# Performance work log

Hardware: AMD Instinct MI355X
Metric: run time of the kernel (lower is better)

The kernel has to match this reference:

```python
import jax, jax.numpy as jnp
import numpy as np

ENCODER_DIM, DECODER_DIM, ATTENTION_DIM = 2048, 512, 512
B, L = 128, 196


def setup_inputs() -> dict:
    key = jax.random.key(0)
    ks = jax.random.split(key, 8)
    s_u = 1.0 / np.sqrt(ENCODER_DIM)
    s_w = 1.0 / np.sqrt(DECODER_DIM)
    s_a = 1.0 / np.sqrt(ATTENTION_DIM)
    return {
        "features": jax.random.normal(ks[0], (B, L, ENCODER_DIM), jnp.float32),
        "hidden_state": jax.random.normal(ks[1], (B, DECODER_DIM), jnp.float32),
        "U_w": jax.random.uniform(ks[2], (ENCODER_DIM, ATTENTION_DIM), jnp.float32, -s_u, s_u),
        "U_b": jax.random.uniform(ks[3], (ATTENTION_DIM,), jnp.float32, -s_u, s_u),
        "W_w": jax.random.uniform(ks[4], (DECODER_DIM, ATTENTION_DIM), jnp.float32, -s_w, s_w),
        "W_b": jax.random.uniform(ks[5], (ATTENTION_DIM,), jnp.float32, -s_w, s_w),
        "A_w": jax.random.uniform(ks[6], (ATTENTION_DIM,), jnp.float32, -s_a, s_a),
        "A_b": jax.random.uniform(ks[7], (1,), jnp.float32, -s_a, s_a),
    }


def reference(features, hidden_state, U_w, U_b, W_w, W_b, A_w, A_b):
    # u_hs: [B, L, A], w_ah: [B, A]
    u_hs = jnp.einsum('ble,ea->bla', features, U_w) + U_b
    w_ah = hidden_state @ W_w + W_b
    combined = jnp.tanh(u_hs + w_ah[:, None, :])          # [B, L, A]
    scores = jnp.einsum('bla,a->bl', combined, A_w) + A_b[0]  # [B, L]
    alpha = jax.nn.softmax(scores, axis=1)                 # [B, L]
    context = jnp.einsum('bl,ble->be', alpha, features)    # [B, E]
    return alpha, context
```

## Files before the change

### kernel.cpp

```cpp
#include <hip/hip_runtime.h>
#include <hip/hip_bf16.h>

#define ENC 2048
#define ADIM 512
#define DEC 512
#define NBATCH 128
#define NL 196
#define MTOT (NBATCH * NL)
#define NKT 32

typedef __attribute__((ext_vector_type(8))) short short8;
typedef __attribute__((ext_vector_type(4))) float f32x4;
typedef __attribute__((ext_vector_type(4))) unsigned int u32x4;

__device__ __forceinline__ unsigned short f2bf(float f) {
    __hip_bfloat16 h = __float2bfloat16(f);
    union { __hip_bfloat16 h; unsigned short u; } cv; cv.h = h; return cv.u;
}
__device__ __forceinline__ unsigned int f2bf2(float lo, float hi) {
    __hip_bfloat162 h = __float22bfloat162_rn(float2{lo, hi});
    union { __hip_bfloat162 h; unsigned int u; } cv; cv.h = h; return cv.u;
}

__device__ __forceinline__ void load_lds16(const void* g, void* l) {
    __builtin_amdgcn_global_load_lds(
        (const __attribute__((address_space(1))) unsigned int*)g,
        (__attribute__((address_space(3))) unsigned int*)l, 16, 0, 0);
}

__global__ void wah_kernel(const float* __restrict__ hidden, const float* __restrict__ Ww,
                           const float* __restrict__ Wb, float* __restrict__ wah) {
    __shared__ __align__(16) float hs[DEC];
    const int b = blockIdx.x, a = threadIdx.x;
    hs[a] = hidden[b * DEC + a];
    __syncthreads();
    float acc = Wb[a];
    #pragma unroll 4
    for (int d = 0; d < DEC; d += 4) {
        f32x4 h = *(const f32x4*)&hs[d];
        acc += h.x * Ww[(d    ) * ADIM + a];
        acc += h.y * Ww[(d + 1) * ADIM + a];
        acc += h.z * Ww[(d + 2) * ADIM + a];
        acc += h.w * Ww[(d + 3) * ADIM + a];
    }
    wah[b * ADIM + a] = acc;
}

__global__ void transpose_uw(const float* __restrict__ Uw, unsigned short* __restrict__ uwT) {
    __shared__ float t[32][33];
    const int k0 = blockIdx.x * 32, n0 = blockIdx.y * 32;
    const int tx = threadIdx.x, ty = threadIdx.y;
    #pragma unroll
    for (int i = 0; i < 4; ++i)
        t[ty + 8 * i][tx] = Uw[(size_t)(k0 + ty + 8 * i) * ADIM + n0 + tx];
    __syncthreads();
    #pragma unroll
    for (int i = 0; i < 4; ++i)
        uwT[(size_t)(n0 + ty + 8 * i) * ENC + k0 + tx] = f2bf(t[tx][ty + 8 * i]);
}

__global__ __launch_bounds__(256, 3) void gemm_score(
    const float* __restrict__ feat, const unsigned short* __restrict__ uwT,
    const float* __restrict__ Ub, const float* __restrict__ wahb,
    const float* __restrict__ Aw, float* __restrict__ part)
{
    __shared__ __align__(16) unsigned char As[32768];
    __shared__ __align__(16) unsigned char Bs[16384];

    const int tid  = threadIdx.x;
    const int lane = tid & 63;
    const int w    = tid >> 6;
    const int wr   = w >> 1, wc = w & 1;
    const int l15  = lane & 15, ldr = lane >> 4;

    const int bid  = blockIdx.x;
    const int work = (bid & 7) * 98 + (bid >> 3);
    const int mb   = work >> 2;
    const int nbk  = work & 3;

    const float* aS[8];
    #pragma unroll
    for (int c = 0; c < 8; ++c) {
        const int rowc = c * 4 + ldr;
        const int sslot = l15 ^ (rowc & 15);
        aS[c] = feat + (size_t)(mb * 128 + w * 32 + rowc) * ENC + sslot * 4;
    }
    const int swzB = ((lane & 7) ^ ((lane >> 3) & 7)) << 3;
    const unsigned short* bS = uwT + (size_t)(nbk * 128 + w * 32 + (lane >> 3)) * ENC + swzB;

    int abyte[4][2][2];
    int bbyte[4][2];
    #pragma unroll
    for (int f = 0; f < 4; ++f) {
        const int ra = wr * 64 + f * 16 + l15;
        const int rb = wc * 64 + f * 16 + l15;
        #pragma unroll
        for (int ks = 0; ks < 2; ++ks) {
            abyte[f][ks][0] = ra * 256 + (((ks * 8 + ldr * 2 + 0) ^ l15) << 4);
            abyte[f][ks][1] = ra * 256 + (((ks * 8 + ldr * 2 + 1) ^ l15) << 4);
            bbyte[f][ks]    = rb * 128 + (((ks * 4 + ldr) ^ (rb & 7)) << 4);
        }
    }

    f32x4 acc[4][4];
    #pragma unroll
    for (int i = 0; i < 4; ++i)
        #pragma unroll
        for (int j = 0; j < 4; ++j)
            acc[i][j] = (f32x4){0.f, 0.f, 0.f, 0.f};

    #pragma unroll 1
    for (int kt = 0; kt < NKT; ++kt) {
        #pragma unroll
        for (int c = 0; c < 8; ++c)
            load_lds16(aS[c] + (size_t)kt * 64, As + w * 8192 + c * 1024);
        #pragma unroll
        for (int c = 0; c < 4; ++c)
            load_lds16(bS + (size_t)kt * 64 + c * 8 * ENC, Bs + w * 4096 + c * 1024);
        __syncthreads();

        #pragma unroll
        for (int ks = 0; ks < 2; ++ks) {
            short8 af[4], bf[4];
            #pragma unroll
            for (int f = 0; f < 4; ++f) {
                f32x4 lo = *(const f32x4*)(As + abyte[f][ks][0]);
                f32x4 hi = *(const f32x4*)(As + abyte[f][ks][1]);
                union { unsigned int u[4]; short8 s; } cv;
                cv.u[0] = f2bf2(lo.x, lo.y);
                cv.u[1] = f2bf2(lo.z, lo.w);
                cv.u[2] = f2bf2(hi.x, hi.y);
                cv.u[3] = f2bf2(hi.z, hi.w);
                af[f] = cv.s;
                bf[f] = *(const short8*)(Bs + bbyte[f][ks]);
            }
            #pragma unroll
            for (int fm = 0; fm < 4; ++fm)
                #pragma unroll
                for (int fn = 0; fn < 4; ++fn)
                    acc[fm][fn] = __builtin_amdgcn_mfma_f32_16x16x32_bf16(
                        af[fm], bf[fn], acc[fm][fn], 0, 0, 0);
        }
        __syncthreads();
    }

    float ub4[4], aw4[4]; int cidx[4];
    #pragma unroll
    for (int f = 0; f < 4; ++f) {
        const int c = nbk * 128 + wc * 64 + f * 16 + l15;
        cidx[f] = c; ub4[f] = Ub[c]; aw4[f] = Aw[c];
    }
    #pragma unroll
    for (int fm = 0; fm < 4; ++fm) {
        #pragma unroll
        for (int r = 0; r < 4; ++r) {
            const int m = mb * 128 + wr * 64 + fm * 16 + ldr * 4 + r;
            const int b = m / NL;
            const float* wrow = wahb + b * ADIM;
            float s = 0.f;
            #pragma unroll
            for (int f = 0; f < 4; ++f)
                s += aw4[f] * tanhf(acc[fm][f][r] + ub4[f] + wrow[cidx[f]]);
            s += __shfl_xor(s, 1);
            s += __shfl_xor(s, 2);
            s += __shfl_xor(s, 4);
            s += __shfl_xor(s, 8);
            if (l15 == 0) part[(nbk * 2 + wc) * MTOT + m] = s;
        }
    }
}

__global__ void softmax_kernel(const float* __restrict__ part, const float* __restrict__ Ab,
                               float* __restrict__ alpha) {
    const int b = blockIdx.x, t = threadIdx.x;
    float sv = 0.f;
    if (t < NL) {
        sv = Ab[0];
        #pragma unroll
        for (int p = 0; p < 8; ++p) sv += part[p * MTOT + b * NL + t];
    }
    float v = (t < NL) ? sv : -3.4e38f;
    #pragma unroll
    for (int o = 32; o >= 1; o >>= 1) v = fmaxf(v, __shfl_xor(v, o));
    __shared__ float rm[4], rs[4];
    if ((t & 63) == 0) rm[t >> 6] = v;
    __syncthreads();
    const float bm = fmaxf(fmaxf(rm[0], rm[1]), fmaxf(rm[2], rm[3]));
    const float e = (t < NL) ? expf(sv - bm) : 0.f;
    float s = e;
    #pragma unroll
    for (int o = 32; o >= 1; o >>= 1) s += __shfl_xor(s, o);
    if ((t & 63) == 0) rs[t >> 6] = s;
    __syncthreads();
    const float bs = rs[0] + rs[1] + rs[2] + rs[3];
    if (t < NL) alpha[b * NL + t] = e / bs;
}

__global__ void context_kernel(const float* __restrict__ feat, const float* __restrict__ alpha,
                               float* __restrict__ ctx) {
    __shared__ float al[NL];
    const int b = blockIdx.x, chunk = blockIdx.y, t = threadIdx.x;
    for (int i = t; i < NL; i += 128) al[i] = alpha[b * NL + i];
    __syncthreads();
    const int e0 = chunk * 512 + t * 4;
    const float* fp = feat + (size_t)b * NL * ENC + e0;
    f32x4 acc0 = (f32x4){0.f, 0.f, 0.f, 0.f};
    f32x4 acc1 = (f32x4){0.f, 0.f, 0.f, 0.f};
    #pragma unroll 2
    for (int l = 0; l < NL; l += 2) {
        f32x4 f0 = *(const f32x4*)(fp + (size_t)l * ENC);
        f32x4 f1 = *(const f32x4*)(fp + (size_t)(l + 1) * ENC);
        acc0 += al[l] * f0;
        acc1 += al[l + 1] * f1;
    }
    f32x4 rsum = acc0 + acc1;
    *(f32x4*)(ctx + (size_t)b * ENC + e0) = rsum;
}

extern "C" void kernel_launch(void* const* d_in, const int* in_sizes, int n_in,
                              void* d_out, int out_size, void* d_ws, size_t ws_size,
                              hipStream_t stream) {
    const float* feat   = (const float*)d_in[0];
    const float* hidden = (const float*)d_in[1];
    const float* Uw     = (const float*)d_in[2];
    const float* Ub     = (const float*)d_in[3];
    const float* Ww     = (const float*)d_in[4];
    const float* Wb     = (const float*)d_in[5];
    const float* Aw     = (const float*)d_in[6];
    const float* Ab     = (const float*)d_in[7];

    float* out   = (float*)d_out;
    float* alpha = out;
    float* ctx   = out + MTOT;

    char* ws = (char*)d_ws;
    float*          wahb  = (float*)ws;
    unsigned short* uwT   = (unsigned short*)(ws + 262144);
    float*          partb = (float*)(ws + 262144 + 2097152);

    wah_kernel<<<dim3(128), dim3(512), 0, stream>>>(hidden, Ww, Wb, wahb);
    transpose_uw<<<dim3(64, 16), dim3(32, 8), 0, stream>>>(Uw, uwT);
    gemm_score<<<dim3(784), dim3(256), 0, stream>>>(feat, uwT, Ub, wahb, Aw, partb);
    softmax_kernel<<<dim3(128), dim3(256), 0, stream>>>(partb, Ab, alpha);
    context_kernel<<<dim3(128, 4), dim3(128), 0, stream>>>(feat, alpha, ctx);
}
```

Before: 187.7 us.

## Compute full attention width per block to read features once

The score GEMM now uses 512-thread blocks that each cover all 512 attention columns for 128 rows, instead of four blocks per row tile. This removes the fourfold re-reading and fp32-to-bf16 conversion of the feature rows. The per-column partial scores are reduced in shared memory, so the softmax reads a single score array. The trade-off is fewer blocks (196) than compute units, larger LDS use and higher accumulator register pressure.

```diff
diff --git a/kernel.cpp b/kernel.cpp
--- a/kernel.cpp
+++ b/kernel.cpp
@@ -59,126 +59,117 @@
         uwT[(size_t)(n0 + ty + 8 * i) * ENC + k0 + tx] = f2bf(t[tx][ty + 8 * i]);
 }
 
-__global__ __launch_bounds__(256, 3) void gemm_score(
+__global__ __launch_bounds__(512, 2) void gemm_score512(
     const float* __restrict__ feat, const unsigned short* __restrict__ uwT,
     const float* __restrict__ Ub, const float* __restrict__ wahb,
-    const float* __restrict__ Aw, float* __restrict__ part)
+    const float* __restrict__ Aw, float* __restrict__ scores)
 {
     __shared__ __align__(16) unsigned char As[32768];
-    __shared__ __align__(16) unsigned char Bs[16384];
+    __shared__ __align__(16) unsigned char Bs[65536];
+    __shared__ float sred[4][128];
 
     const int tid  = threadIdx.x;
     const int lane = tid & 63;
     const int w    = tid >> 6;
-    const int wr   = w >> 1, wc = w & 1;
+    const int wr   = w >> 2;
+    const int wc   = w & 3;
     const int l15  = lane & 15, ldr = lane >> 4;
-
-    const int bid  = blockIdx.x;
-    const int work = (bid & 7) * 98 + (bid >> 3);
-    const int mb   = work >> 2;
-    const int nbk  = work & 3;
-
-    const float* aS[8];
-    #pragma unroll
-    for (int c = 0; c < 8; ++c) {
+    const int mb   = blockIdx.x;
+
+    const float* aS[4];
+    #pragma unroll
+    for (int c = 0; c < 4; ++c) {
         const int rowc = c * 4 + ldr;
-        const int sslot = l15 ^ (rowc & 15);
-        aS[c] = feat + (size_t)(mb * 128 + w * 32 + rowc) * ENC + sslot * 4;
-    }
-    const int swzB = ((lane & 7) ^ ((lane >> 3) & 7)) << 3;
-    const unsigned short* bS = uwT + (size_t)(nbk * 128 + w * 32 + (lane >> 3)) * ENC + swzB;
-
-    int abyte[4][2][2];
-    int bbyte[4][2];
-    #pragma unroll
-    for (int f = 0; f < 4; ++f) {
-        const int ra = wr * 64 + f * 16 + l15;
-        const int rb = wc * 64 + f * 16 + l15;
-        #pragma unroll
-        for (int ks = 0; ks < 2; ++ks) {
-            abyte[f][ks][0] = ra * 256 + (((ks * 8 + ldr * 2 + 0) ^ l15) << 4);
-            abyte[f][ks][1] = ra * 256 + (((ks * 8 + ldr * 2 + 1) ^ l15) << 4);
-            bbyte[f][ks]    = rb * 128 + (((ks * 4 + ldr) ^ (rb & 7)) << 4);
-        }
-    }
-
-    f32x4 acc[4][4];
+        aS[c] = feat + (size_t)(mb * 128 + w * 16 + rowc) * ENC + ((l15 ^ rowc) << 2);
+    }
+    const unsigned short* bS = uwT
+        + (size_t)(w * 64 + (lane >> 3)) * ENC
+        + (((lane & 7) ^ ((lane >> 3) & 7)) << 3);
+
+    f32x4 acc[4][8];
     #pragma unroll
     for (int i = 0; i < 4; ++i)
         #pragma unroll
-        for (int j = 0; j < 4; ++j)
+        for (int j = 0; j < 8; ++j)
             acc[i][j] = (f32x4){0.f, 0.f, 0.f, 0.f};
+
+    const int aRowBase = (wr * 64 + l15) * 256;
+    const int bRowBase = (wc * 128 + l15) * 128;
 
     #pragma unroll 1
     for (int kt = 0; kt < NKT; ++kt) {
         #pragma unroll
+        for (int c = 0; c < 4; ++c)
+            load_lds16(aS[c] + (size_t)kt * 64, As + w * 4096 + c * 1024);
+        #pragma unroll
         for (int c = 0; c < 8; ++c)
-            load_lds16(aS[c] + (size_t)kt * 64, As + w * 8192 + c * 1024);
-        #pragma unroll
-        for (int c = 0; c < 4; ++c)
-            load_lds16(bS + (size_t)kt * 64 + c * 8 * ENC, Bs + w * 4096 + c * 1024);
+            load_lds16(bS + (size_t)kt * 64 + c * 8 * ENC, Bs + w * 8192 + c * 1024);
         __syncthreads();
 
         #pragma unroll
         for (int ks = 0; ks < 2; ++ks) {
-            short8 af[4], bf[4];
+            short8 af[4];
             #pragma unroll
             for (int f = 0; f < 4; ++f) {
-                f32x4 lo = *(const f32x4*)(As + abyte[f][ks][0]);
-                f32x4 hi = *(const f32x4*)(As + abyte[f][ks][1]);
+                const int q0 = (ks * 8 + ldr * 2) ^ l15;
+                const int q1 = (ks * 8 + ldr * 2 + 1) ^ l15;
+                f32x4 lo = *(const f32x4*)(As + aRowBase + f * 4096 + (q0 << 4));
+                f32x4 hi = *(const f32x4*)(As + aRowBase + f * 4096 + (q1 << 4));
                 union { unsigned int u[4]; short8 s; } cv;
                 cv.u[0] = f2bf2(lo.x, lo.y);
                 cv.u[1] = f2bf2(lo.z, lo.w);
                 cv.u[2] = f2bf2(hi.x, hi.y);
                 cv.u[3] = f2bf2(hi.z, hi.w);
                 af[f] = cv.s;
-                bf[f] = *(const short8*)(Bs + bbyte[f][ks]);
             }
+            const int bSlot = (((ks * 4 + ldr) ^ (l15 & 7)) << 4);
             #pragma unroll
-            for (int fm = 0; fm < 4; ++fm)
+            for (int fn = 0; fn < 8; ++fn) {
+                short8 bf = *(const short8*)(Bs + bRowBase + fn * 2048 + bSlot);
                 #pragma unroll
-                for (int fn = 0; fn < 4; ++fn)
+                for (int fm = 0; fm < 4; ++fm)
                     acc[fm][fn] = __builtin_amdgcn_mfma_f32_16x16x32_bf16(
-                        af[fm], bf[fn], acc[fm][fn], 0, 0, 0);
+                        af[fm], bf, acc[fm][fn], 0, 0, 0);
+            }
         }
         __syncthreads();
     }
 
-    float ub4[4], aw4[4]; int cidx[4];
-    #pragma unroll
-    for (int f = 0; f < 4; ++f) {
-        const int c = nbk * 128 + wc * 64 + f * 16 + l15;
-        cidx[f] = c; ub4[f] = Ub[c]; aw4[f] = Aw[c];
+    float ub8[8], aw8[8]; int cidx[8];
+    #pragma unroll
+    for (int fn = 0; fn < 8; ++fn) {
+        const int c = wc * 128 + fn * 16 + l15;
+        cidx[fn] = c; ub8[fn] = Ub[c]; aw8[fn] = Aw[c];
     }
     #pragma unroll
     for (int fm = 0; fm < 4; ++fm) {
         #pragma unroll
         for (int r = 0; r < 4; ++r) {
-            const int m = mb * 128 + wr * 64 + fm * 16 + ldr * 4 + r;
-            const int b = m / NL;
+            const int lr = wr * 64 + fm * 16 + ldr * 4 + r;
+            const int m  = mb * 128 + lr;
+            const int b  = m / NL;
             const float* wrow = wahb + b * ADIM;
             float s = 0.f;
             #pragma unroll
-            for (int f = 0; f < 4; ++f)
-                s += aw4[f] * tanhf(acc[fm][f][r] + ub4[f] + wrow[cidx[f]]);
+            for (int fn = 0; fn < 8; ++fn)
+                s += aw8[fn] * tanhf(acc[fm][fn][r] + ub8[fn] + wrow[cidx[fn]]);
             s += __shfl_xor(s, 1);
             s += __shfl_xor(s, 2);
             s += __shfl_xor(s, 4);
             s += __shfl_xor(s, 8);
-            if (l15 == 0) part[(nbk * 2 + wc) * MTOT + m] = s;
+            if (l15 == 0) sred[wc][lr] = s;
         }
     }
-}
-
-__global__ void softmax_kernel(const float* __restrict__ part, const float* __restrict__ Ab,
+    __syncthreads();
+    if (tid < 128)
+        scores[mb * 128 + tid] = sred[0][tid] + sred[1][tid] + sred[2][tid] + sred[3][tid];
+}
+
+__global__ void softmax_kernel(const float* __restrict__ scores, const float* __restrict__ Ab,
                                float* __restrict__ alpha) {
     const int b = blockIdx.x, t = threadIdx.x;
     float sv = 0.f;
-    if (t < NL) {
-        sv = Ab[0];
-        #pragma unroll
-        for (int p = 0; p < 8; ++p) sv += part[p * MTOT + b * NL + t];
-    }
+    if (t < NL) sv = scores[b * NL + t] + Ab[0];
     float v = (t < NL) ? sv : -3.4e38f;
     #pragma unroll
     for (int o = 32; o >= 1; o >>= 1) v = fmaxf(v, __shfl_xor(v, o));
@@ -234,13 +225,13 @@
     float* ctx   = out + MTOT;
 
     char* ws = (char*)d_ws;
-    float*          wahb  = (float*)ws;
-    unsigned short* uwT   = (unsigned short*)(ws + 262144);
-    float*          partb = (float*)(ws + 262144 + 2097152);
+    float*          wahb   = (float*)ws;
+    unsigned short* uwT    = (unsigned short*)(ws + 262144);
+    float*          scores = (float*)(ws + 262144 + 2097152);
 
     wah_kernel<<<dim3(128), dim3(512), 0, stream>>>(hidden, Ww, Wb, wahb);
     transpose_uw<<<dim3(64, 16), dim3(32, 8), 0, stream>>>(Uw, uwT);
-    gemm_score<<<dim3(784), dim3(256), 0, stream>>>(feat, uwT, Ub, wahb, Aw, partb);
-    softmax_kernel<<<dim3(128), dim3(256), 0, stream>>>(partb, Ab, alpha);
+    gemm_score512<<<dim3(196), dim3(512), 0, stream>>>(feat, uwT, Ub, wahb, Aw, scores);
+    softmax_kernel<<<dim3(128), dim3(256), 0, stream>>>(scores, Ab, alpha);
     context_kernel<<<dim3(128, 4), dim3(128), 0, stream>>>(feat, alpha, ctx);
 }
```

New measurement: 167.7 us. -10.7%, faster.

## Pre-convert features to bf16 and double-buffer the score GEMM pipeline

Applied to the files above, without the earlier changes.

Adds a pass that converts the feature tensor to bf16 once, so the score GEMM loads bf16 directly into LDS instead of converting fp32 per tile. The GEMM is restructured into a two-stage double-buffered K loop with smaller LDS tiles and higher occupancy. The context reduction reads the bf16 copy, halving its bytes but lowering its precision. The extra conversion pass adds a full read plus half-size write of features, and the context kernel launches fewer blocks.

```diff
diff --git a/kernel.cpp b/kernel.cpp
--- a/kernel.cpp
+++ b/kernel.cpp
@@ -7,7 +7,7 @@
 #define NBATCH 128
 #define NL 196
 #define MTOT (NBATCH * NL)
-#define NKT 32
+#define NK32 64
 
 typedef __attribute__((ext_vector_type(8))) short short8;
 typedef __attribute__((ext_vector_type(4))) float f32x4;
@@ -20,12 +20,29 @@
 __device__ __forceinline__ unsigned int f2bf2(float lo, float hi) {
     __hip_bfloat162 h = __float22bfloat162_rn(float2{lo, hi});
     union { __hip_bfloat162 h; unsigned int u; } cv; cv.h = h; return cv.u;
+}
+__device__ __forceinline__ float bf2f(unsigned short u) {
+    union { unsigned int u; float f; } cv; cv.u = ((unsigned int)u) << 16; return cv.f;
 }
 
 __device__ __forceinline__ void load_lds16(const void* g, void* l) {
     __builtin_amdgcn_global_load_lds(
         (const __attribute__((address_space(1))) unsigned int*)g,
         (__attribute__((address_space(3))) unsigned int*)l, 16, 0, 0);
+}
+
+__global__ void cvt_feat_kernel(const float* __restrict__ feat, unsigned short* __restrict__ featb) {
+    const size_t total  = (size_t)MTOT * ENC;
+    const size_t stride = (size_t)gridDim.x * blockDim.x * 8;
+    size_t i = ((size_t)blockIdx.x * blockDim.x + threadIdx.x) * 8;
+    for (; i < total; i += stride) {
+        f32x4 lo = *(const f32x4*)(feat + i);
+        f32x4 hi = *(const f32x4*)(feat + i + 4);
+        u32x4 v;
+        v.x = f2bf2(lo.x, lo.y); v.y = f2bf2(lo.z, lo.w);
+        v.z = f2bf2(hi.x, hi.y); v.w = f2bf2(hi.z, hi.w);
+        *(u32x4*)(featb + i) = v;
+    }
 }
 
 __global__ void wah_kernel(const float* __restrict__ hidden, const float* __restrict__ Ww,
@@ -59,13 +76,15 @@
         uwT[(size_t)(n0 + ty + 8 * i) * ENC + k0 + tx] = f2bf(t[tx][ty + 8 * i]);
 }
 
-__global__ __launch_bounds__(256, 3) void gemm_score(
-    const float* __restrict__ feat, const unsigned short* __restrict__ uwT,
+__global__ __launch_bounds__(256, 4) void gemm_score_2ph(
+    const unsigned short* __restrict__ featb, const unsigned short* __restrict__ uwT,
     const float* __restrict__ Ub, const float* __restrict__ wahb,
     const float* __restrict__ Aw, float* __restrict__ part)
 {
-    __shared__ __align__(16) unsigned char As[32768];
-    __shared__ __align__(16) unsigned char Bs[16384];
+    __shared__ __align__(16) unsigned char Ab0[8192];
+    __shared__ __align__(16) unsigned char Ab1[8192];
+    __shared__ __align__(16) unsigned char Bb0[8192];
+    __shared__ __align__(16) unsigned char Bb1[8192];
 
     const int tid  = threadIdx.x;
     const int lane = tid & 63;
@@ -78,28 +97,19 @@
     const int mb   = work >> 2;
     const int nbk  = work & 3;
 
-    const float* aS[8];
-    #pragma unroll
-    for (int c = 0; c < 8; ++c) {
-        const int rowc = c * 4 + ldr;
-        const int sslot = l15 ^ (rowc & 15);
-        aS[c] = feat + (size_t)(mb * 128 + w * 32 + rowc) * ENC + sslot * 4;
-    }
-    const int swzB = ((lane & 7) ^ ((lane >> 3) & 7)) << 3;
-    const unsigned short* bS = uwT + (size_t)(nbk * 128 + w * 32 + (lane >> 3)) * ENC + swzB;
-
-    int abyte[4][2][2];
-    int bbyte[4][2];
+    const int srow  = lane >> 2;
+    const int sslot = (lane & 3) ^ ((lane >> 3) & 3);
+    const unsigned short* aS = featb + (size_t)(mb  * 128 + w * 32 + srow) * ENC + sslot * 8;
+    const unsigned short* bS = uwT   + (size_t)(nbk * 128 + w * 32 + srow) * ENC + sslot * 8;
+
+    const int rs = (l15 >> 1) & 3;
+    int abyte[4], bbyte[4];
     #pragma unroll
     for (int f = 0; f < 4; ++f) {
         const int ra = wr * 64 + f * 16 + l15;
         const int rb = wc * 64 + f * 16 + l15;
-        #pragma unroll
-        for (int ks = 0; ks < 2; ++ks) {
-            abyte[f][ks][0] = ra * 256 + (((ks * 8 + ldr * 2 + 0) ^ l15) << 4);
-            abyte[f][ks][1] = ra * 256 + (((ks * 8 + ldr * 2 + 1) ^ l15) << 4);
-            bbyte[f][ks]    = rb * 128 + (((ks * 4 + ldr) ^ (rb & 7)) << 4);
-        }
+        abyte[f] = ra * 64 + ((ldr ^ rs) << 4);
+        bbyte[f] = rb * 64 + ((ldr ^ rs) << 4);
     }
 
     f32x4 acc[4][4];
@@ -109,40 +119,47 @@
         for (int j = 0; j < 4; ++j)
             acc[i][j] = (f32x4){0.f, 0.f, 0.f, 0.f};
 
+#define STAGE(KT, AB, BB) {                                                   \
+    _Pragma("unroll")                                                         \
+    for (int c = 0; c < 2; ++c) {                                             \
+        load_lds16(aS + (size_t)(KT) * 32 + c * 16 * ENC,                     \
+                   (AB) + w * 2048 + c * 1024);                               \
+        load_lds16(bS + (size_t)(KT) * 32 + c * 16 * ENC,                     \
+                   (BB) + w * 2048 + c * 1024);                               \
+    }                                                                         \
+    __builtin_amdgcn_sched_barrier(0);                                        \
+}
+#define COMPUTE(AB, BB) {                                                     \
+    short8 af[4], bf[4];                                                      \
+    _Pragma("unroll")                                                         \
+    for (int f = 0; f < 4; ++f) {                                             \
+        af[f] = *(const short8*)((AB) + abyte[f]);                            \
+        bf[f] = *(const short8*)((BB) + bbyte[f]);                            \
+    }                                                                         \
+    __builtin_amdgcn_s_setprio(1);                                            \
+    _Pragma("unroll")                                                         \
+    for (int fm = 0; fm < 4; ++fm)                                            \
+        _Pragma("unroll")                                                     \
+        for (int fn = 0; fn < 4; ++fn)                                        \
+            acc[fm][fn] = __builtin_amdgcn_mfma_f32_16x16x32_bf16(            \
+                af[fm], bf[fn], acc[fm][fn], 0, 0, 0);                        \
+    __builtin_amdgcn_s_setprio(0);                                            \
+}
+
+    STAGE(0, Ab0, Bb0);
+    __syncthreads();
     #pragma unroll 1
-    for (int kt = 0; kt < NKT; ++kt) {
-        #pragma unroll
-        for (int c = 0; c < 8; ++c)
-            load_lds16(aS[c] + (size_t)kt * 64, As + w * 8192 + c * 1024);
-        #pragma unroll
-        for (int c = 0; c < 4; ++c)
-            load_lds16(bS + (size_t)kt * 64 + c * 8 * ENC, Bs + w * 4096 + c * 1024);
+    for (int kt = 0; kt < NK32; kt += 2) {
+        STAGE(kt + 1, Ab1, Bb1);
+        COMPUTE(Ab0, Bb0);
         __syncthreads();
-
-        #pragma unroll
-        for (int ks = 0; ks < 2; ++ks) {
-            short8 af[4], bf[4];
-            #pragma unroll
-            for (int f = 0; f < 4; ++f) {
-                f32x4 lo = *(const f32x4*)(As + abyte[f][ks][0]);
-                f32x4 hi = *(const f32x4*)(As + abyte[f][ks][1]);
-                union { unsigned int u[4]; short8 s; } cv;
-                cv.u[0] = f2bf2(lo.x, lo.y);
-                cv.u[1] = f2bf2(lo.z, lo.w);
-                cv.u[2] = f2bf2(hi.x, hi.y);
-                cv.u[3] = f2bf2(hi.z, hi.w);
-                af[f] = cv.s;
-                bf[f] = *(const short8*)(Bs + bbyte[f][ks]);
-            }
-            #pragma unroll
-            for (int fm = 0; fm < 4; ++fm)
-                #pragma unroll
-                for (int fn = 0; fn < 4; ++fn)
-                    acc[fm][fn] = __builtin_amdgcn_mfma_f32_16x16x32_bf16(
-                        af[fm], bf[fn], acc[fm][fn], 0, 0, 0);
-        }
+        const int k2 = (kt + 2 < NK32) ? kt + 2 : NK32 - 1;
+        STAGE(k2, Ab0, Bb0);
+        COMPUTE(Ab1, Bb1);
         __syncthreads();
     }
+#undef STAGE
+#undef COMPUTE
 
     float ub4[4], aw4[4]; int cidx[4];
     #pragma unroll
@@ -196,25 +213,32 @@
     if (t < NL) alpha[b * NL + t] = e / bs;
 }
 
-__global__ void context_kernel(const float* __restrict__ feat, const float* __restrict__ alpha,
-                               float* __restrict__ ctx) {
+__global__ void context_bf16_kernel(const unsigned short* __restrict__ featb,
+                                    const float* __restrict__ alpha, float* __restrict__ ctx) {
     __shared__ float al[NL];
     const int b = blockIdx.x, chunk = blockIdx.y, t = threadIdx.x;
     for (int i = t; i < NL; i += 128) al[i] = alpha[b * NL + i];
     __syncthreads();
-    const int e0 = chunk * 512 + t * 4;
-    const float* fp = feat + (size_t)b * NL * ENC + e0;
-    f32x4 acc0 = (f32x4){0.f, 0.f, 0.f, 0.f};
-    f32x4 acc1 = (f32x4){0.f, 0.f, 0.f, 0.f};
-    #pragma unroll 2
-    for (int l = 0; l < NL; l += 2) {
-        f32x4 f0 = *(const f32x4*)(fp + (size_t)l * ENC);
-        f32x4 f1 = *(const f32x4*)(fp + (size_t)(l + 1) * ENC);
-        acc0 += al[l] * f0;
-        acc1 += al[l + 1] * f1;
-    }
-    f32x4 rsum = acc0 + acc1;
-    *(f32x4*)(ctx + (size_t)b * ENC + e0) = rsum;
+    const int e0 = chunk * 1024 + t * 8;
+    const unsigned short* fp = featb + (size_t)b * NL * ENC + e0;
+    float a0=0.f,a1=0.f,a2=0.f,a3=0.f,a4=0.f,a5=0.f,a6=0.f,a7=0.f;
+    for (int l = 0; l < NL; ++l) {
+        short8 v = *(const short8*)(fp + (size_t)l * ENC);
+        const float sc = al[l];
+        a0 += sc * bf2f((unsigned short)v[0]);
+        a1 += sc * bf2f((unsigned short)v[1]);
+        a2 += sc * bf2f((unsigned short)v[2]);
+        a3 += sc * bf2f((unsigned short)v[3]);
+        a4 += sc * bf2f((unsigned short)v[4]);
+        a5 += sc * bf2f((unsigned short)v[5]);
+        a6 += sc * bf2f((unsigned short)v[6]);
+        a7 += sc * bf2f((unsigned short)v[7]);
+    }
+    float* cp = ctx + (size_t)b * ENC + e0;
+    f32x4 r0 = (f32x4){a0, a1, a2, a3};
+    f32x4 r1 = (f32x4){a4, a5, a6, a7};
+    *(f32x4*)cp = r0;
+    *(f32x4*)(cp + 4) = r1;
 }
 
 extern "C" void kernel_launch(void* const* d_in, const int* in_sizes, int n_in,
@@ -233,14 +257,18 @@
     float* alpha = out;
     float* ctx   = out + MTOT;
 
+    const size_t FEATB_BYTES = (size_t)MTOT * ENC * 2;
+
     char* ws = (char*)d_ws;
-    float*          wahb  = (float*)ws;
-    unsigned short* uwT   = (unsigned short*)(ws + 262144);
-    float*          partb = (float*)(ws + 262144 + 2097152);
-
+    unsigned short* featb = (unsigned short*)ws;
+    float*          wahb  = (float*)(ws + FEATB_BYTES);
+    unsigned short* uwT   = (unsigned short*)(ws + FEATB_BYTES + 262144);
+    float*          partb = (float*)(ws + FEATB_BYTES + 262144 + 2097152);
+
+    cvt_feat_kernel<<<dim3(2048), dim3(256), 0, stream>>>(feat, featb);
     wah_kernel<<<dim3(128), dim3(512), 0, stream>>>(hidden, Ww, Wb, wahb);
     transpose_uw<<<dim3(64, 16), dim3(32, 8), 0, stream>>>(Uw, uwT);
-    gemm_score<<<dim3(784), dim3(256), 0, stream>>>(feat, uwT, Ub, wahb, Aw, partb);
+    gemm_score_2ph<<<dim3(784), dim3(256), 0, stream>>>(featb, uwT, Ub, wahb, Aw, partb);
     softmax_kernel<<<dim3(128), dim3(256), 0, stream>>>(partb, Ab, alpha);
-    context_kernel<<<dim3(128, 4), dim3(128), 0, stream>>>(feat, alpha, ctx);
-}
+    context_bf16_kernel<<<dim3(128, 2), dim3(128), 0, stream>>>(featb, alpha, ctx);
+}
```

New measurement: 172.3 us. 8.2% less time.
